# Performance work log

Hardware: AMD Instinct MI355X
Metric: run time of the kernel (lower is better)

## Reference

```python
import jax, jax.numpy as jnp
import numpy as np

EPS = 1e-5

def layer_norm(x, g, b):
    mu = jnp.mean(x, axis=-1, keepdims=True)
    var = jnp.var(x, axis=-1, keepdims=True)
    return (x - mu) * jax.lax.rsqrt(var + EPS) * g + b

def setup_inputs() -> dict:
    key = jax.random.key(0)
    ks = jax.random.split(key, 12)
    B, N, D, H = 32, 577, 768, 12
    Dh = D // H
    hid = 4 * D
    s = lambda d: 1.0 / np.sqrt(d)
    return {
        "x": jax.random.normal(ks[0], (B, N, D), jnp.float32),
        "ln1_g": jnp.ones((D,), jnp.float32),
        "ln1_b": jnp.zeros((D,), jnp.float32),
        "ln2_g": jnp.ones((D,), jnp.float32),
        "ln2_b": jnp.zeros((D,), jnp.float32),
        "w_qkv": jax.random.normal(ks[1], (D, 3 * D), jnp.float32) * s(D),
        "b_qkv": jnp.zeros((3 * D,), jnp.float32),
        "w_proj": jax.random.normal(ks[2], (D, D), jnp.float32) * s(D),
        "b_proj": jnp.zeros((D,), jnp.float32),
        "w_fc1": jax.random.normal(ks[3], (D, hid), jnp.float32) * s(D),
        "b_fc1": jnp.zeros((hid,), jnp.float32),
        "w_fc2": jax.random.normal(ks[4], (hid, D), jnp.float32) * s(hid),
        "b_fc2": jnp.zeros((D,), jnp.float32),
    }

def reference(x, ln1_g, ln1_b, ln2_g, ln2_b, w_qkv, b_qkv, w_proj, b_proj,
              w_fc1, b_fc1, w_fc2, b_fc2):
    B, N, D = x.shape
    H = 12
    Dh = D // H
    scale = Dh ** -0.5
    # --- attention branch ---
    h = layer_norm(x, ln1_g, ln1_b)
    qkv = h @ w_qkv + b_qkv                      # [B, N, 3D]
    qkv = qkv.reshape(B, N, 3, H, Dh).transpose(2, 0, 3, 1, 4)  # [3, B, H, N, Dh]
    q, k, v = qkv[0], qkv[1], qkv[2]
    attn = jnp.einsum('bhnd,bhmd->bhnm', q, k) * scale  # [B, H, N, N]
    attn = jax.nn.softmax(attn, axis=-1)
    o = jnp.einsum('bhnm,bhmd->bhnd', attn, v)           # [B, H, N, Dh]
    o = o.transpose(0, 2, 1, 3).reshape(B, N, D)
    o = o @ w_proj + b_proj
    x = x + o
    # --- MLP branch ---
    h = layer_norm(x, ln2_g, ln2_b)
    h = jnp.clip(h @ w_fc1 + b_fc1, 0.0, 6.0)            # ReLU6
    h = h @ w_fc2 + b_fc2
    return x + h
```

## Files before the change

kernel.cpp:

```cpp
#include <hip/hip_runtime.h>
#include <math.h>


typedef unsigned short u16;
typedef _Float16 f16;
typedef __attribute__((ext_vector_type(8))) _Float16 f16x8;
typedef __attribute__((ext_vector_type(4))) float f32x4;

__device__ __forceinline__ u16 f2h(float x) {
    union { f16 h; u16 u; } cv;
    cv.h = (f16)x;
    return cv.u;
}
__device__ __forceinline__ float h2f(u16 b) {
    union { u16 u; f16 h; } cv;
    cv.u = b;
    return (float)cv.h;
}
__device__ __forceinline__ void load_lds16(const u16* g, void* l) {
    __builtin_amdgcn_global_load_lds(
        (const __attribute__((address_space(1))) void*)g,
        (__attribute__((address_space(3))) void*)l, 16, 0, 0);
}
__device__ __forceinline__ int xcd_swz(int lid, int nwg) {
    const int x = lid & 7, pos = lid >> 3;
    const int q = nwg >> 3, r = nwg & 7;
    return (x < r ? x * (q + 1) : r * (q + 1) + (x - r) * q) + pos;
}

__global__ __launch_bounds__(256)
void wprep_kernel(const float* __restrict__ W, u16* __restrict__ Th,
                  int K, int N)
{
    __shared__ float t[32][33];
    const int n0 = blockIdx.x * 32, k0 = blockIdx.y * 32;
    const int tr = threadIdx.x >> 3, tc4 = (threadIdx.x & 7) * 4;
    const float4 v = *(const float4*)&W[(size_t)(k0 + tr) * N + n0 + tc4];
    t[tr][tc4 + 0] = v.x; t[tr][tc4 + 1] = v.y;
    t[tr][tc4 + 2] = v.z; t[tr][tc4 + 3] = v.w;
    __syncthreads();
    ushort4 h;
    h.x = f2h(t[tc4 + 0][tr]);
    h.y = f2h(t[tc4 + 1][tr]);
    h.z = f2h(t[tc4 + 2][tr]);
    h.w = f2h(t[tc4 + 3][tr]);
    *(ushort4*)&Th[(size_t)(n0 + tr) * K + k0 + tc4] = h;
}

__global__ __launch_bounds__(256)
void ln_kernel(const float* __restrict__ x, const float* __restrict__ g,
               const float* __restrict__ beta, u16* __restrict__ oh, int pad)
{
    const int row = blockIdx.x;
    const int tid = threadIdx.x;
    const float* xr = x + (size_t)row * 768;
    const float v0 = xr[tid], v1 = xr[tid + 256], v2 = xr[tid + 512];
    float s  = v0 + v1 + v2;
    float ss = v0 * v0 + v1 * v1 + v2 * v2;
    #pragma unroll
    for (int off = 1; off < 64; off <<= 1) {
        s  += __shfl_xor(s, off);
        ss += __shfl_xor(ss, off);
    }
    __shared__ float redS[4], redQ[4];
    const int wid = tid >> 6;
    if ((tid & 63) == 0) { redS[wid] = s; redQ[wid] = ss; }
    __syncthreads();
    s  = redS[0] + redS[1] + redS[2] + redS[3];
    ss = redQ[0] + redQ[1] + redQ[2] + redQ[3];
    const float mean = s * (1.0f / 768.0f);
    const float var  = ss * (1.0f / 768.0f) - mean * mean;
    const float rstd = rsqrtf(var + 1e-5f);
    int row_p = row;
    if (pad) {
        const unsigned bb = (unsigned)row / 577u;
        row_p = (int)(bb * 640u + ((unsigned)row - bb * 577u));
    }
    u16* ohr = oh + (size_t)row_p * 768;
    #pragma unroll
    for (int u = 0; u < 3; ++u) {
        const int c = tid + u * 256;
        const float vv = (u == 0) ? v0 : (u == 1) ? v1 : v2;
        ohr[c] = f2h((vv - mean) * rstd * g[c] + beta[c]);
    }
}

template<int RELU6, int RES, int OMODE, int PADMAP>
__global__ __launch_bounds__(512, 2)
void mfma_gemm(const u16* __restrict__ Ah, const u16* __restrict__ Bh,
               const float* __restrict__ bias, const float* res,
               float* Cf, u16* __restrict__ Ch,
               u16* __restrict__ Qh_, u16* __restrict__ Kh_,
               u16* __restrict__ Vth_,
               int M, int N, int K)
{
    __shared__ u16 lds[34816];

    const int tid  = threadIdx.x;
    const int wid  = tid >> 6;
    const int lane = tid & 63;
    const int wr = wid >> 2;
    const int wc = wid & 3;

    const int nwg = gridDim.x * gridDim.y;
    int lid = blockIdx.y * gridDim.x + blockIdx.x;
    lid = xcd_swz(lid, nwg);
    const int bm = (lid / gridDim.x) * 256;
    const int bn = (lid % gridDim.x) * 256;

    const int trow = tid >> 2;
    const int c    = tid & 3;
    const u16* pA[2]; const u16* pB[2];
    char* dA[2]; char* dB[2];
    char* ldsb = (char*)lds;
    #pragma unroll
    for (int i = 0; i < 2; ++i) {
        const int r = i * 128 + trow;
        const int kg = c ^ ((r >> 1) & 3);
        pA[i] = Ah + (size_t)(bm + r) * K + kg * 8;
        pB[i] = Bh + (size_t)(bn + r) * K + kg * 8;
        dA[i] = ldsb +         i * 8192 + wid * 1024;
        dB[i] = ldsb + 16384 + i * 8192 + wid * 1024;
    }

    const int l15 = lane & 15;
    const int lg  = lane >> 4;

    f32x4 acc[8][4] = {};
    const int np = K >> 5;

    #pragma unroll
    for (int i = 0; i < 2; ++i) {
        load_lds16(pA[i], dA[i]); load_lds16(pB[i], dB[i]);
        pA[i] += 32; pB[i] += 32;
    }

    int cur = 0;
    for (int p = 0; p < np; ++p) {
        asm volatile("s_waitcnt vmcnt(0)" ::: "memory");
        __builtin_amdgcn_s_barrier();
        if (p + 1 < np) {
            const int o = (cur ^ 1) * 32768;
            #pragma unroll
            for (int i = 0; i < 2; ++i) {
                load_lds16(pA[i], dA[i] + o); load_lds16(pB[i], dB[i] + o);
                pA[i] += 32; pB[i] += 32;
            }
        }
        const u16* sA = lds + cur * 16384;
        const u16* sB = sA + 8192;

        f16x8 ah[8];
        #pragma unroll
        for (int fm = 0; fm < 8; ++fm) {
            const int ar = wr * 128 + fm * 16 + l15;
            const int pc = lg ^ ((ar >> 1) & 3);
            ah[fm] = *(const f16x8*)&sA[ar * 32 + pc * 8];
        }
        #pragma unroll
        for (int fn = 0; fn < 4; ++fn) {
            const int br = wc * 64 + fn * 16 + l15;
            const int pc = lg ^ ((br >> 1) & 3);
            const f16x8 bh = *(const f16x8*)&sB[br * 32 + pc * 8];
            #pragma unroll
            for (int fm = 0; fm < 8; ++fm)
                acc[fm][fn] = __builtin_amdgcn_mfma_f32_16x16x32_f16(
                    ah[fm], bh, acc[fm][fn], 0, 0, 0);
        }
        cur ^= 1;
    }

    __syncthreads();

    if (OMODE == 2) {
        const int s  = bn / 768;
        const int hh = ((bn + wc * 64) - s * 768) >> 6;
        u16* eph = lds + wid * 4352;
        #pragma unroll
        for (int h = 0; h < 2; ++h) {
            #pragma unroll
            for (int fn = 0; fn < 4; ++fn) {
                const float bv = bias[bn + wc * 64 + fn * 16 + l15];
                #pragma unroll
                for (int f2 = 0; f2 < 4; ++f2) {
                    const f32x4 v = acc[h * 4 + f2][fn];
                    #pragma unroll
                    for (int j = 0; j < 4; ++j) {
                        const float o = v[j] + bv;
                        const int idx = (s == 2)
                            ? (fn * 16 + l15) * 68 + f2 * 16 + lg * 4 + j
                            : (f2 * 16 + lg * 4 + j) * 68 + fn * 16 + l15;
                        eph[idx] = f2h(o);
                    }
                }
            }
            const int gr0 = bm + wr * 128 + h * 64;
            const int bb  = gr0 / 640;
            const int n0  = gr0 - bb * 640;
            if (s == 2) {
                u16* dh = Vth_ + (size_t)(bb * 12 + hh) * 64 * 640 + n0 + lane;
                #pragma unroll 8
                for (int d = 0; d < 64; ++d)
                    dh[(size_t)d * 640] = eph[d * 68 + lane];
            } else {
                u16* base = ((s == 0) ? Qh_ : Kh_) +
                            ((size_t)(bb * 12 + hh) * 640 + n0) * 64 + lane;
                #pragma unroll 8
                for (int rr = 0; rr < 64; ++rr)
                    base[(size_t)rr * 64] = eph[rr * 68 + lane];
            }
        }
    } else if (OMODE == 1) {
        u16* eph = lds + wid * 4352;
        const int cc0 = bn + wc * 64;
        #pragma unroll
        for (int h = 0; h < 2; ++h) {
            #pragma unroll
            for (int fn = 0; fn < 4; ++fn) {
                const float bv = bias[cc0 + fn * 16 + l15];
                #pragma unroll
                for (int f2 = 0; f2 < 4; ++f2) {
                    const f32x4 v = acc[h * 4 + f2][fn];
                    #pragma unroll
                    for (int j = 0; j < 4; ++j) {
                        float o = v[j] + bv;
                        if (RELU6) o = fminf(fmaxf(o, 0.0f), 6.0f);
                        eph[(f2 * 16 + lg * 4 + j) * 68 + fn * 16 + l15] = f2h(o);
                    }
                }
            }
            #pragma unroll 8
            for (int rr = 0; rr < 64; ++rr) {
                const int r = bm + wr * 128 + h * 64 + rr;
                if (r < M)
                    Ch[(size_t)r * N + cc0 + lane] = eph[rr * 68 + lane];
            }
        }
    } else {
        float* epf = (float*)lds + wid * (32 * 68);
        const int cc0 = bn + wc * 64;
        #pragma unroll
        for (int h = 0; h < 4; ++h) {
            #pragma unroll
            for (int fn = 0; fn < 4; ++fn) {
                const float bv = bias[cc0 + fn * 16 + l15];
                #pragma unroll
                for (int f2 = 0; f2 < 2; ++f2) {
                    const f32x4 v = acc[h * 2 + f2][fn];
                    #pragma unroll
                    for (int j = 0; j < 4; ++j) {
                        float o = v[j] + bv;
                        if (RELU6) o = fminf(fmaxf(o, 0.0f), 6.0f);
                        epf[(f2 * 16 + lg * 4 + j) * 68 + fn * 16 + l15] = o;
                    }
                }
            }
            #pragma unroll 8
            for (int rr = 0; rr < 32; ++rr) {
                const int r = bm + wr * 128 + h * 32 + rr;
                float o = epf[rr * 68 + lane];
                if (PADMAP) {
                    const int bb2 = r / 640;
                    const int nn = r - bb2 * 640;
                    if (nn < 577) {
                        const size_t ro = (size_t)(bb2 * 577 + nn) * N + cc0 + lane;
                        if (RES) o += res[ro];
                        Cf[ro] = o;
                    }
                } else if (r < M) {
                    const size_t ro = (size_t)r * N + cc0 + lane;
                    if (RES) o += res[ro];
                    Cf[ro] = o;
                }
            }
        }
    }
}

__global__ __launch_bounds__(256)
void attn_mfma(const u16* __restrict__ Qh, const u16* __restrict__ Kh,
               const u16* __restrict__ Vth, u16* __restrict__ Oh)
{
    constexpr int SEQ = 577, NP = 640;
    __shared__ u16 sK[2 * 4096], sV[2 * 4096];
    __shared__ u16 sPh[4][16 * 72];

    const int tid  = threadIdx.x;
    const int wave = tid >> 6;
    const int lane = tid & 63;
    const int l15 = lane & 15, lg = lane >> 4;

    const int nwg = gridDim.x * gridDim.y;
    int lid = blockIdx.y * gridDim.x + blockIdx.x;
    lid = xcd_swz(lid, nwg);
    const int q0 = (lid % gridDim.x) * 64;
    const int bh = lid / gridDim.x;

    const size_t qkBase = (size_t)bh * NP * 64;
    const size_t vBase  = (size_t)bh * 64 * NP;

    f16x8 qfh[2];
    {
        const size_t ro = qkBase + (size_t)(q0 + wave * 16 + l15) * 64;
        #pragma unroll
        for (int ks = 0; ks < 2; ++ks)
            qfh[ks] = *(const f16x8*)&Qh[ro + (ks * 4 + lg) * 8];
    }

    const int srow = lane >> 3;
    const int sc   = lane & 7;

    f32x4 oacc[4] = {};
    float mrun = -1e30f, lrun = 0.0f;
    constexpr int NT = 10;

    #pragma unroll
    for (int t = 0; t < 2; ++t) {
        const int row = wave * 16 + t * 8 + srow;
        const int lc  = sc ^ (row & 7);
        load_lds16(Kh + qkBase + (size_t)row * 64 + lc * 8,
                   (char*)sK + wave * 2048 + t * 1024);
        load_lds16(Vth + vBase + (size_t)row * NP + lc * 8,
                   (char*)sV + wave * 2048 + t * 1024);
    }
    __syncthreads();

    int cur = 0;
    for (int it = 0; it < NT; ++it) {
        const int kv0 = it * 64;
        if (it + 1 < NT) {
            const int nkv = kv0 + 64;
            const int o = (cur ^ 1) * 8192;
            #pragma unroll
            for (int t = 0; t < 2; ++t) {
                const int row = wave * 16 + t * 8 + srow;
                const int lc  = sc ^ (row & 7);
                load_lds16(Kh + qkBase + (size_t)(nkv + row) * 64 + lc * 8,
                           (char*)sK + o + wave * 2048 + t * 1024);
                load_lds16(Vth + vBase + (size_t)row * NP + nkv + lc * 8,
                           (char*)sV + o + wave * 2048 + t * 1024);
            }
        }
        const u16* sKc = sK + cur * 4096;
        const u16* sVc = sV + cur * 4096;

        f32x4 sacc[4] = {};
        __builtin_amdgcn_s_setprio(1);
        #pragma unroll
        for (int fkv = 0; fkv < 4; ++fkv) {
            const int row = fkv * 16 + l15;
            #pragma unroll
            for (int ks = 0; ks < 2; ++ks) {
                const int ph = ((ks * 4 + lg) ^ (row & 7)) * 8;
                const f16x8 kh = *(const f16x8*)&sKc[row * 64 + ph];
                sacc[fkv] = __builtin_amdgcn_mfma_f32_16x16x32_f16(
                    kh, qfh[ks], sacc[fkv], 0, 0, 0);
            }
        }
        __builtin_amdgcn_s_setprio(0);

        float p[4][4];
        float mt = -1e30f;
        const bool tail = (kv0 + 64 > SEQ);
        #pragma unroll
        for (int fkv = 0; fkv < 4; ++fkv)
            #pragma unroll
            for (int j = 0; j < 4; ++j) {
                float sv = sacc[fkv][j] * 0.125f;
                if (tail && (kv0 + fkv * 16 + lg * 4 + j >= SEQ)) sv = -1e30f;
                p[fkv][j] = sv;
                mt = fmaxf(mt, sv);
            }
        mt = fmaxf(mt, __shfl_xor(mt, 16));
        mt = fmaxf(mt, __shfl_xor(mt, 32));
        const float mnew = fmaxf(mrun, mt);
        const float corr = __expf(mrun - mnew);
        float rs = 0.0f;
        #pragma unroll
        for (int fkv = 0; fkv < 4; ++fkv)
            #pragma unroll
            for (int j = 0; j < 4; ++j) {
                p[fkv][j] = __expf(p[fkv][j] - mnew);
                rs += p[fkv][j];
            }
        rs += __shfl_xor(rs, 16);
        rs += __shfl_xor(rs, 32);
        lrun = lrun * corr + rs;
        mrun = mnew;
        #pragma unroll
        for (int fd = 0; fd < 4; ++fd)
            #pragma unroll
            for (int j = 0; j < 4; ++j) oacc[fd][j] *= corr;

        u16* phr = &sPh[wave][l15 * 72];
        #pragma unroll
        for (int fkv = 0; fkv < 4; ++fkv) {
            ushort4 hv;
            hv.x = f2h(p[fkv][0]);
            hv.y = f2h(p[fkv][1]);
            hv.z = f2h(p[fkv][2]);
            hv.w = f2h(p[fkv][3]);
            *(ushort4*)&phr[fkv * 16 + lg * 4] = hv;
        }

        __builtin_amdgcn_s_setprio(1);
        #pragma unroll
        for (int ks = 0; ks < 2; ++ks) {
            const f16x8 pbh = *(const f16x8*)&sPh[wave][l15 * 72 + (ks * 4 + lg) * 8];
            #pragma unroll
            for (int fd = 0; fd < 4; ++fd) {
                const int row = fd * 16 + l15;
                const int ph = ((ks * 4 + lg) ^ (row & 7)) * 8;
                const f16x8 vh = *(const f16x8*)&sVc[row * 64 + ph];
                oacc[fd] = __builtin_amdgcn_mfma_f32_16x16x32_f16(
                    vh, pbh, oacc[fd], 0, 0, 0);
            }
        }
        __builtin_amdgcn_s_setprio(0);

        __syncthreads();
        cur ^= 1;
    }

    {
        const float inv = 1.0f / lrun;
        const int b = bh / 12, h = bh % 12;
        u16* ep = &sPh[wave][0];
        #pragma unroll
        for (int fd = 0; fd < 4; ++fd) {
            ushort4 hv;
            hv.x = f2h(oacc[fd][0] * inv);
            hv.y = f2h(oacc[fd][1] * inv);
            hv.z = f2h(oacc[fd][2] * inv);
            hv.w = f2h(oacc[fd][3] * inv);
            *(ushort4*)&ep[l15 * 68 + fd * 16 + lg * 4] = hv;
        }
        #pragma unroll 4
        for (int rr = 0; rr < 16; ++rr) {
            const int q = q0 + wave * 16 + rr;
            if (q < SEQ)
                Oh[((size_t)(b * 640 + q)) * 768 + h * 64 + lane] =
                    ep[rr * 68 + lane];
        }
    }
}

extern "C" void kernel_launch(void* const* d_in, const int* in_sizes, int n_in,
                              void* d_out, int out_size, void* d_ws, size_t ws_size,
                              hipStream_t stream)
{
    const float* x      = (const float*)d_in[0];
    const float* ln1_g  = (const float*)d_in[1];
    const float* ln1_b  = (const float*)d_in[2];
    const float* ln2_g  = (const float*)d_in[3];
    const float* ln2_b  = (const float*)d_in[4];
    const float* w_qkv  = (const float*)d_in[5];
    const float* b_qkv  = (const float*)d_in[6];
    const float* w_proj = (const float*)d_in[7];
    const float* b_proj = (const float*)d_in[8];
    const float* w_fc1  = (const float*)d_in[9];
    const float* b_fc1  = (const float*)d_in[10];
    const float* w_fc2  = (const float*)d_in[11];
    const float* b_fc2  = (const float*)d_in[12];
    float* out = (float*)d_out;

    const int M  = 18464;
    const int Mq = 20480;
    const int Mf = 18688;

    char* p = (char*)d_ws;
    u16* Wqkv  = (u16*)p;    p += (size_t)2304 * 768 * 2;
    u16* Wproj = (u16*)p;    p += (size_t)768 * 768 * 2;
    u16* Wfc1  = (u16*)p;    p += (size_t)3072 * 768 * 2;
    u16* Wfc2  = (u16*)p;    p += (size_t)768 * 3072 * 2;
    u16* A_h = (u16*)p;      p += (size_t)Mq * 768 * 2;
    u16* Qh  = (u16*)p;      p += (size_t)384 * 640 * 64 * 2;
    u16* Kh  = (u16*)p;      p += (size_t)384 * 640 * 64 * 2;
    u16* Vth = (u16*)p;      p += (size_t)384 * 64 * 640 * 2;
    u16* fc1h = (u16*)p;     p += (size_t)Mf * 3072 * 2;

    wprep_kernel<<<dim3(72, 24),  256, 0, stream>>>(w_qkv,  Wqkv,  768, 2304);
    wprep_kernel<<<dim3(24, 24),  256, 0, stream>>>(w_proj, Wproj, 768, 768);
    wprep_kernel<<<dim3(96, 24),  256, 0, stream>>>(w_fc1,  Wfc1,  768, 3072);
    wprep_kernel<<<dim3(24, 96),  256, 0, stream>>>(w_fc2,  Wfc2,  3072, 768);

    ln_kernel<<<M, 256, 0, stream>>>(x, ln1_g, ln1_b, A_h, 1);
    mfma_gemm<0, 0, 2, 0><<<dim3(9, 80), 512, 0, stream>>>(
        A_h, Wqkv, b_qkv, nullptr, nullptr, nullptr,
        Qh, Kh, Vth, Mq, 2304, 768);
    attn_mfma<<<dim3(10, 384), 256, 0, stream>>>(Qh, Kh, Vth, A_h);
    mfma_gemm<0, 1, 0, 1><<<dim3(3, 80), 512, 0, stream>>>(
        A_h, Wproj, b_proj, x, out, nullptr,
        nullptr, nullptr, nullptr, Mq, 768, 768);
    ln_kernel<<<M, 256, 0, stream>>>(out, ln2_g, ln2_b, A_h, 0);
    mfma_gemm<1, 0, 1, 0><<<dim3(12, 73), 512, 0, stream>>>(
        A_h, Wfc1, b_fc1, nullptr, nullptr, fc1h,
        nullptr, nullptr, nullptr, M, 3072, 768);
    mfma_gemm<0, 1, 0, 0><<<dim3(3, 73), 512, 0, stream>>>(
        fc1h, Wfc2, b_fc2, out, out, nullptr,
        nullptr, nullptr, nullptr, M, 768, 3072);
}
```

Before: 600.9 us.

## Deepen GEMM LDS pipeline to four stages with partial vmcnt waits

The GEMM main loop moves from a double-buffered LDS scheme to a four-slot ring that prefetches three K-steps ahead. Each iteration waits with vmcnt(8) or vmcnt(4) rather than draining all loads, which hides more global-load latency. The MFMA section is also wrapped in s_setprio to favour math waves. The cost is LDS growing to 128KB per block, which with launch_bounds(512,2) may leave room for only one block per CU and reduce occupancy.

```diff
diff --git a/kernel.cpp b/kernel.cpp
--- a/kernel.cpp
+++ b/kernel.cpp
@@ -94,7 +94,7 @@
                u16* __restrict__ Vth_,
                int M, int N, int K)
 {
-    __shared__ u16 lds[34816];
+    __shared__ u16 lds[65536];
 
     const int tid  = threadIdx.x;
     const int wid  = tid >> 6;
@@ -127,29 +127,31 @@
     const int lg  = lane >> 4;
 
     f32x4 acc[8][4] = {};
-    const int np = K >> 5;
+    const int nh = K >> 5;
 
     #pragma unroll
-    for (int i = 0; i < 2; ++i) {
-        load_lds16(pA[i], dA[i]); load_lds16(pB[i], dB[i]);
-        pA[i] += 32; pB[i] += 32;
-    }
-
-    int cur = 0;
-    for (int p = 0; p < np; ++p) {
-        asm volatile("s_waitcnt vmcnt(0)" ::: "memory");
+    for (int s = 0; s < 3; ++s) {
+        const int o = s << 15;
+        load_lds16(pA[0], dA[0] + o); load_lds16(pA[1], dA[1] + o);
+        load_lds16(pB[0], dB[0] + o); load_lds16(pB[1], dB[1] + o);
+        pA[0] += 32; pA[1] += 32; pB[0] += 32; pB[1] += 32;
+    }
+
+    for (int h = 0; h < nh; ++h) {
+        if (h + 2 < nh)      asm volatile("s_waitcnt vmcnt(8)" ::: "memory");
+        else if (h + 1 < nh) asm volatile("s_waitcnt vmcnt(4)" ::: "memory");
+        else                 asm volatile("s_waitcnt vmcnt(0)" ::: "memory");
         __builtin_amdgcn_s_barrier();
-        if (p + 1 < np) {
-            const int o = (cur ^ 1) * 32768;
-            #pragma unroll
-            for (int i = 0; i < 2; ++i) {
-                load_lds16(pA[i], dA[i] + o); load_lds16(pB[i], dB[i] + o);
-                pA[i] += 32; pB[i] += 32;
-            }
-        }
-        const u16* sA = lds + cur * 16384;
+        if (h + 3 < nh) {
+            const int o = ((h + 3) & 3) << 15;
+            load_lds16(pA[0], dA[0] + o); load_lds16(pA[1], dA[1] + o);
+            load_lds16(pB[0], dB[0] + o); load_lds16(pB[1], dB[1] + o);
+            pA[0] += 32; pA[1] += 32; pB[0] += 32; pB[1] += 32;
+        }
+        const u16* sA = lds + ((h & 3) << 14);
         const u16* sB = sA + 8192;
 
+        __builtin_amdgcn_s_setprio(1);
         f16x8 ah[8];
         #pragma unroll
         for (int fm = 0; fm < 8; ++fm) {
@@ -167,7 +169,7 @@
                 acc[fm][fn] = __builtin_amdgcn_mfma_f32_16x16x32_f16(
                     ah[fm], bh, acc[fm][fn], 0, 0, 0);
         }
-        cur ^= 1;
+        __builtin_amdgcn_s_setprio(0);
     }
 
     __syncthreads();
```

New measurement: 591.5 us. Within noise of the previous version (-1.6%).
